# Performance work log

Hardware: AMD Instinct MI355X
Metric: run time of the kernel (lower is better)

The kernel has to match this reference:

```python
import jax, jax.numpy as jnp
import numpy as np

V, DW, D, H, F, N = 50272, 512, 1024, 16, 4096, 4   # vocab, word_embed_proj_dim, hidden, heads, ffn, layers
B, L = 4, 1024
T = B * L
MAX_POS = 2048


def layernorm(x, w, b, eps=1e-5):
    m = jnp.mean(x, axis=-1, keepdims=True)
    v = jnp.mean((x - m) ** 2, axis=-1, keepdims=True)
    return (x - m) * jax.lax.rsqrt(v + eps) * w + b


def setup_inputs() -> dict:
    key = jax.random.key(0)
    ks = jax.random.split(key, 16)
    s = 0.02
    inp = {
        "input_ids": jax.random.randint(ks[0], (T,), 0, V),
        "positions": jnp.tile(jnp.arange(L), B),          # per-sequence positions 0..L-1
        "offsets": (jnp.arange(B) + 1) * L,               # cumulative sequence ends
        "cache_indices": jnp.arange(T),
        "k_cache": jnp.zeros((N, T, D), jnp.float32),
        "v_cache": jnp.zeros((N, T, D), jnp.float32),
        "embed_w": jax.random.normal(ks[1], (V, DW)) * s,
        "pos_w": jax.random.normal(ks[2], (MAX_POS + 2, D)) * s,
        "proj_in_w": jax.random.normal(ks[3], (D, DW)) * s,
        "proj_out_w": jax.random.normal(ks[4], (DW, D)) * s,
        "ln1_w": jnp.ones((N, D)), "ln1_b": jnp.zeros((N, D)),
        "qw": jax.random.normal(ks[5], (N, D, D)) * s, "qb": jnp.zeros((N, D)),
        "kw": jax.random.normal(ks[6], (N, D, D)) * s, "kb": jnp.zeros((N, D)),
        "vw": jax.random.normal(ks[7], (N, D, D)) * s, "vb": jnp.zeros((N, D)),
        "ow": jax.random.normal(ks[8], (N, D, D)) * s, "ob": jnp.zeros((N, D)),
        "fc1w": jax.random.normal(ks[9], (N, F, D)) * s, "fc1b": jnp.zeros((N, F)),
        "fc2w": jax.random.normal(ks[10], (N, D, F)) * s, "fc2b": jnp.zeros((N, D)),
        "ln2_w": jnp.ones((N, D)), "ln2_b": jnp.zeros((N, D)),
    }
    return inp


def reference(input_ids, positions, offsets, cache_indices, k_cache, v_cache,
              embed_w, pos_w, proj_in_w, proj_out_w,
              ln1_w, ln1_b, qw, qb, kw, kb, vw, vb, ow, ob,
              fc1w, fc1b, fc2w, fc2b, ln2_w, ln2_b):
    # prompt_init=True path: fresh causal varlen attention over packed equal-length sequences.
    hd = D // H
    scale = hd ** -0.5
    emb = embed_w[input_ids] @ proj_in_w.T            # [T, D] (proj_in since DW != D)
    pos = pos_w[positions + 2]                        # learned pos emb with offset 2
    h = (emb + pos).reshape(B, L, D)
    causal = jnp.tril(jnp.ones((L, L), bool))

    def step(h, p):
        l1w, l1b, Wq, bq, Wk, bk, Wv, bv, Wo, bo, W1, b1, W2, b2, l2w, l2b = p
        r = h                                          # post-LN (do_layer_norm_before=False)
        q = (h @ Wq.T + bq).reshape(B, L, H, hd)
        k = (h @ Wk.T + bk).reshape(B, L, H, hd)
        v = (h @ Wv.T + bv).reshape(B, L, H, hd)
        s = jnp.einsum('bqhd,bkhd->bhqk', q * scale, k)
        s = jnp.where(causal, s, -1e9)
        pa = jax.nn.softmax(s, axis=-1)
        o = jnp.einsum('bhqk,bkhd->bqhd', pa, v).reshape(B, L, D)
        h = layernorm(r + (o @ Wo.T + bo), l1w, l1b)
        r = h
        h = jax.nn.relu(h @ W1.T + b1)
        h = h @ W2.T + b2
        h = layernorm(r + h, l2w, l2b)
        return h, None

    h, _ = jax.lax.scan(step, h, (ln1_w, ln1_b, qw, qb, kw, kb, vw, vb, ow, ob,
                                  fc1w, fc1b, fc2w, fc2b, ln2_w, ln2_b))
    # no decoder final_layer_norm when do_layer_norm_before=False
    h = h.reshape(T, D) @ proj_out_w.T                # [T, DW]
    last = h[offsets - 1]                             # last token of each sequence [B, DW]
    return last @ embed_w.T                           # logits [B, V]
```

## Files before the change

### kernel.cpp

```cpp
#include <hip/hip_runtime.h>
#include <stdint.h>

typedef _Float16 f16;
typedef __attribute__((ext_vector_type(8))) _Float16 f16x8;
typedef __attribute__((ext_vector_type(4))) _Float16 f16x4;
typedef __attribute__((ext_vector_type(4))) float f32x4;

constexpr int kT = 4096;
constexpr int kD = 1024;
constexpr int kDW = 512;
constexpr int kF = 4096;
constexpr int kV = 50272;

__device__ __forceinline__ void gload16(const void* g, void* lbase, int lane) {
#if __has_builtin(__builtin_amdgcn_global_load_lds)
  __builtin_amdgcn_global_load_lds((const __attribute__((address_space(1))) void*)g,
                                   (__attribute__((address_space(3))) void*)lbase, 16, 0, 0);
#else
  *(f16x8*)((char*)lbase + lane * 16) = *(const f16x8*)g;
#endif
}

__global__ __launch_bounds__(512, 4) void gemm_p8(
    const f16* __restrict__ A, const f16* __restrict__ W,
    const float* __restrict__ bias, void* __restrict__ Cv,
    int M, int N, int K, int ldc, int flags, int S)
{
  __shared__ f16 LA[2][128 * 64];
  __shared__ f16 LB[2][128 * 64];
  const int tid = threadIdx.x, lane = tid & 63, wv = tid >> 6;
  const int nby = M >> 7;
  const int nb = nby * (N >> 7);
  int id = blockIdx.x;
  id = (id & 7) * ((int)gridDim.x >> 3) + (id >> 3);
  const int s = id / nb;
  const int r = id - s * nb;
  const int bx = r / nby, by = r - bx * nby;
  const int row0 = by * 128, col0 = bx * 128;
  const int klen = K / S, koff = s * klen;
  const int wm = (wv >> 1) * 32, wn = (wv & 1) * 64;
  const int l15 = lane & 15, l4 = lane >> 4;

  f32x4 acc[2][4] = {};

  const int srow = wv * 16 + (lane >> 3);
  const int schunk = ((lane & 7) ^ (lane >> 3)) * 8;
  const f16* Ag = A + (size_t)(row0 + srow) * K + koff + schunk;
  const f16* Wg = W + (size_t)(col0 + srow) * K + koff + schunk;
  const int lrow = wv * 16;

  const int nt = klen >> 6;
#pragma unroll
  for (int j = 0; j < 2; ++j) {
    gload16(Ag + (size_t)j * 8 * K, &LA[0][(lrow + j * 8) * 64], lane);
    gload16(Wg + (size_t)j * 8 * K, &LB[0][(lrow + j * 8) * 64], lane);
  }

  for (int t = 0; t < nt; ++t) {
    const int cur = t & 1;
    if (t + 1 < nt) {
      const size_t ko = (size_t)(t + 1) * 64;
#pragma unroll
      for (int j = 0; j < 2; ++j) {
        gload16(Ag + (size_t)j * 8 * K + ko, &LA[cur ^ 1][(lrow + j * 8) * 64], lane);
        gload16(Wg + (size_t)j * 8 * K + ko, &LB[cur ^ 1][(lrow + j * 8) * 64], lane);
      }
      asm volatile("s_waitcnt vmcnt(4)" ::: "memory");
    } else {
      asm volatile("s_waitcnt vmcnt(0)" ::: "memory");
    }
    __builtin_amdgcn_s_barrier();

    f16x8 af[2][2], bf[2][4];
#pragma unroll
    for (int ks = 0; ks < 2; ++ks) {
#pragma unroll
      for (int mr = 0; mr < 2; ++mr) {
        const int rowa = wm + mr * 16 + l15;
        af[ks][mr] = *(const f16x8*)&LA[cur][rowa * 64 + (((ks * 4 + l4) ^ (rowa & 7)) * 8)];
      }
#pragma unroll
      for (int nr = 0; nr < 4; ++nr) {
        const int rowb = wn + nr * 16 + l15;
        bf[ks][nr] = *(const f16x8*)&LB[cur][rowb * 64 + (((ks * 4 + l4) ^ (rowb & 7)) * 8)];
      }
    }
#pragma unroll
    for (int mr = 0; mr < 2; ++mr)
#pragma unroll
      for (int nr = 0; nr < 4; ++nr) {
        acc[mr][nr] = __builtin_amdgcn_mfma_f32_16x16x32_f16(af[0][mr], bf[0][nr], acc[mr][nr], 0, 0, 0);
        acc[mr][nr] = __builtin_amdgcn_mfma_f32_16x16x32_f16(af[1][mr], bf[1][nr], acc[mr][nr], 0, 0, 0);
      }
    __builtin_amdgcn_sched_barrier(0);
    __builtin_amdgcn_s_barrier();
  }

  const bool relu = (flags & 1) != 0;
  const bool outf = (flags & 2) != 0;
  const bool ph16 = (flags & 4) != 0;
  float* Cf = (float*)Cv + (size_t)s * M * ldc;
  f16* Cp = (f16*)Cv + (size_t)s * M * ldc;
  f16* Ch = (f16*)Cv;
  const float* bs = (s == 0) ? bias : nullptr;
#pragma unroll
  for (int nr = 0; nr < 4; ++nr) {
    const int col = col0 + wn + nr * 16 + l15;
    const float bv = bs ? bs[col] : 0.f;
#pragma unroll
    for (int mr = 0; mr < 2; ++mr) {
#pragma unroll
      for (int rr = 0; rr < 4; ++rr) {
        const int row = row0 + wm + mr * 16 + l4 * 4 + rr;
        float v = acc[mr][nr][rr] + bv;
        if (relu) v = fmaxf(v, 0.f);
        if (ph16)      Cp[(size_t)row * ldc + col] = (f16)v;
        else if (outf) Cf[(size_t)row * ldc + col] = v;
        else           Ch[(size_t)row * ldc + col] = (f16)v;
      }
    }
  }
}

__global__ __launch_bounds__(256) void gemm_f16(
    const f16* __restrict__ A, const float* __restrict__ W,
    const float* __restrict__ bias, void* __restrict__ Cv,
    int M, int N, int K, int ldc, int flags)
{
  __shared__ f16 As[128][40];
  __shared__ f16 Ws[128][40];
  const int tid = threadIdx.x;
  const int lane = tid & 63;
  const int wid = tid >> 6;
  const int row0 = blockIdx.y * 128, col0 = blockIdx.x * 128;
  const int wm = (wid >> 1) * 64, wn = (wid & 1) * 64;
  const int l15 = lane & 15, k8 = (lane >> 4) * 8;
  const int lr = tid >> 2, lc8 = (tid & 3) * 8;

  f32x4 acc[4][4] = {};

  const f16* Ap = A + (size_t)(row0 + lr) * K + lc8;
  const float* Wp = W + (size_t)(col0 + lr) * K + lc8;

  for (int k0 = 0; k0 < K; k0 += 32) {
    f16x8 a0 = *(const f16x8*)(Ap + k0);
    f16x8 a1 = *(const f16x8*)(Ap + (size_t)64 * K + k0);
    f32x4 w00 = *(const f32x4*)(Wp + k0);
    f32x4 w01 = *(const f32x4*)(Wp + k0 + 4);
    f32x4 w10 = *(const f32x4*)(Wp + (size_t)64 * K + k0);
    f32x4 w11 = *(const f32x4*)(Wp + (size_t)64 * K + k0 + 4);
    f16x8 wv0, wv1;
#pragma unroll
    for (int j = 0; j < 4; ++j) {
      wv0[j] = (f16)w00[j]; wv0[4 + j] = (f16)w01[j];
      wv1[j] = (f16)w10[j]; wv1[4 + j] = (f16)w11[j];
    }
    __syncthreads();
    *(f16x8*)&As[lr][lc8] = a0;
    *(f16x8*)&As[lr + 64][lc8] = a1;
    *(f16x8*)&Ws[lr][lc8] = wv0;
    *(f16x8*)&Ws[lr + 64][lc8] = wv1;
    __syncthreads();
    f16x8 af[4], bfr[4];
#pragma unroll
    for (int r = 0; r < 4; ++r) af[r] = *(const f16x8*)&As[wm + r * 16 + l15][k8];
#pragma unroll
    for (int r = 0; r < 4; ++r) bfr[r] = *(const f16x8*)&Ws[wn + r * 16 + l15][k8];
#pragma unroll
    for (int mr = 0; mr < 4; ++mr)
#pragma unroll
      for (int nr = 0; nr < 4; ++nr)
        acc[mr][nr] = __builtin_amdgcn_mfma_f32_16x16x32_f16(af[mr], bfr[nr], acc[mr][nr], 0, 0, 0);
  }

  const bool relu = (flags & 1) != 0;
  const bool outf = (flags & 2) != 0;
  float* Cf = (float*)Cv;
  f16* Ch = (f16*)Cv;
#pragma unroll
  for (int nr = 0; nr < 4; ++nr) {
    const int col = col0 + wn + nr * 16 + l15;
    const float bv = bias ? bias[col] : 0.f;
#pragma unroll
    for (int mr = 0; mr < 4; ++mr) {
#pragma unroll
      for (int r = 0; r < 4; ++r) {
        const int row = row0 + wm + mr * 16 + (lane >> 4) * 4 + r;
        float v = acc[mr][nr][r] + bv;
        if (relu) v = fmaxf(v, 0.f);
        if (outf) Cf[(size_t)row * ldc + col] = v;
        else      Ch[(size_t)row * ldc + col] = (f16)v;
      }
    }
  }
}

__global__ __launch_bounds__(256) void attn_mfma4(const f16* __restrict__ qkv,
                                                  f16* __restrict__ out)
{
  __shared__ f16 Ks[64][72];
  __shared__ f16 Vt[64][72];
  __shared__ f16 Ps[4][32][72];
  const int qt = blockIdx.x, h = blockIdx.y, b = blockIdx.z;
  const int tid = threadIdx.x, lane = tid & 63, wv = tid >> 6;
  const int l15 = lane & 15, l4 = lane >> 4;
  constexpr float kC1 = 0.18033688f;
  constexpr float kC2 = -11.5415603f;

  f16x8 qa[2][2];
#pragma unroll
  for (int mr = 0; mr < 2; ++mr) {
    const size_t qrow = (size_t)(b * 1024 + qt * 128 + wv * 32 + mr * 16 + l15);
#pragma unroll
    for (int ks = 0; ks < 2; ++ks)
      qa[mr][ks] = *(const f16x8*)(qkv + qrow * 3072 + h * 64 + ks * 32 + l4 * 8);
  }

  float l[2][4] = {};
  f32x4 o[2][4] = {};

  const int skey = tid >> 2;
  const int spart = (tid & 3) * 16;
  const int vxor = (skey >> 3) ^ (tid & 3);
  const int vcol = vxor * 8 + (skey & 7);
  const int qmin = qt * 128 + wv * 32;
  const int ntiles = 2 * qt + 2;

  f16x8 kk0, kk1, vv0, vv1;
  {
    const f16* kvb = qkv + (size_t)(b * 1024 + skey) * 3072 + h * 64;
    kk0 = *(const f16x8*)(kvb + 1024 + spart);
    kk1 = *(const f16x8*)(kvb + 1024 + spart + 8);
    vv0 = *(const f16x8*)(kvb + 2048 + spart);
    vv1 = *(const f16x8*)(kvb + 2048 + spart + 8);
  }

  for (int kt = 0; kt < ntiles; ++kt) {
    *(f16x8*)&Ks[skey][spart] = kk0;
    *(f16x8*)&Ks[skey][spart + 8] = kk1;
#pragma unroll
    for (int j = 0; j < 8; ++j) {
      Vt[spart + j][vcol] = vv0[j];
      Vt[spart + 8 + j][vcol] = vv1[j];
    }
    __syncthreads();
    if (kt + 1 < ntiles) {
      const f16* kvb = qkv + (size_t)(b * 1024 + (kt + 1) * 64 + skey) * 3072 + h * 64;
      kk0 = *(const f16x8*)(kvb + 1024 + spart);
      kk1 = *(const f16x8*)(kvb + 1024 + spart + 8);
      vv0 = *(const f16x8*)(kvb + 2048 + spart);
      vv1 = *(const f16x8*)(kvb + 2048 + spart + 8);
    }

    if (kt * 64 <= qmin + 31) {
      f32x4 s[2][4] = {};
#pragma unroll
      for (int f = 0; f < 4; ++f) {
        f16x8 kb0 = *(const f16x8*)&Ks[f * 16 + l15][l4 * 8];
        f16x8 kb1 = *(const f16x8*)&Ks[f * 16 + l15][32 + l4 * 8];
#pragma unroll
        for (int mr = 0; mr < 2; ++mr) {
          s[mr][f] = __builtin_amdgcn_mfma_f32_16x16x32_f16(qa[mr][0], kb0, s[mr][f], 0, 0, 0);
          s[mr][f] = __builtin_amdgcn_mfma_f32_16x16x32_f16(qa[mr][1], kb1, s[mr][f], 0, 0, 0);
        }
      }
#pragma unroll
      for (int mr = 0; mr < 2; ++mr) {
        float sc[4][4];
        const bool needmask = (kt * 64 + 63) > (qmin + mr * 16);
        if (needmask) {
#pragma unroll
          for (int f = 0; f < 4; ++f)
#pragma unroll
            for (int r = 0; r < 4; ++r) {
              const int qg = qmin + mr * 16 + l4 * 4 + r;
              const int kg = kt * 64 + f * 16 + l15;
              sc[f][r] = (kg <= qg) ? exp2f(fmaf(s[mr][f][r], kC1, kC2)) : 0.f;
            }
        } else {
#pragma unroll
          for (int f = 0; f < 4; ++f)
#pragma unroll
            for (int r = 0; r < 4; ++r)
              sc[f][r] = exp2f(fmaf(s[mr][f][r], kC1, kC2));
        }
#pragma unroll
        for (int r = 0; r < 4; ++r)
          l[mr][r] += (sc[0][r] + sc[1][r]) + (sc[2][r] + sc[3][r]);
#pragma unroll
        for (int f = 0; f < 4; ++f)
#pragma unroll
          for (int r = 0; r < 4; ++r)
            Ps[wv][mr * 16 + l4 * 4 + r][f * 16 + l15] = (f16)sc[f][r];
      }
      f16x8 pa[2][2];
#pragma unroll
      for (int mr = 0; mr < 2; ++mr)
#pragma unroll
        for (int ks = 0; ks < 2; ++ks)
          pa[mr][ks] = *(const f16x8*)&Ps[wv][mr * 16 + l15][ks * 32 + l4 * 8];
#pragma unroll
      for (int hf = 0; hf < 4; ++hf) {
        f16x8 vb0 = *(const f16x8*)&Vt[hf * 16 + l15][((l4) ^ hf) * 8];
        f16x8 vb1 = *(const f16x8*)&Vt[hf * 16 + l15][((4 + l4) ^ hf) * 8];
#pragma unroll
        for (int mr = 0; mr < 2; ++mr) {
          o[mr][hf] = __builtin_amdgcn_mfma_f32_16x16x32_f16(pa[mr][0], vb0, o[mr][hf], 0, 0, 0);
          o[mr][hf] = __builtin_amdgcn_mfma_f32_16x16x32_f16(pa[mr][1], vb1, o[mr][hf], 0, 0, 0);
        }
      }
    }
    __syncthreads();
  }

#pragma unroll
  for (int mr = 0; mr < 2; ++mr) {
    float inv[4];
#pragma unroll
    for (int r = 0; r < 4; ++r) {
      float L = l[mr][r];
      L += __shfl_xor(L, 1);
      L += __shfl_xor(L, 2);
      L += __shfl_xor(L, 4);
      L += __shfl_xor(L, 8);
      inv[r] = 1.f / L;
    }
    f16* dst = out + (size_t)(b * 1024 + qt * 128 + wv * 32 + mr * 16 + l4 * 4) * 1024 + h * 64 + l15;
#pragma unroll
    for (int hf = 0; hf < 4; ++hf)
#pragma unroll
      for (int r = 0; r < 4; ++r)
        dst[(size_t)r * 1024 + hf * 16] = (f16)(o[mr][hf][r] * inv[r]);
  }
}

__device__ __forceinline__ void ln_body(f32x4 v, const float* w, const float* bvec,
                                        float* O32, f16* Oh, size_t base, int tid)
{
  float sm = v[0] + v[1] + v[2] + v[3];
  float sq = v[0] * v[0] + v[1] * v[1] + v[2] * v[2] + v[3] * v[3];
#pragma unroll
  for (int msk = 32; msk; msk >>= 1) { sm += __shfl_xor(sm, msk); sq += __shfl_xor(sq, msk); }
  __shared__ float sb[4], qb_[4];
  const int wid = tid >> 6, lane = tid & 63;
  if (lane == 0) { sb[wid] = sm; qb_[wid] = sq; }
  __syncthreads();
  sm = sb[0] + sb[1] + sb[2] + sb[3];
  sq = qb_[0] + qb_[1] + qb_[2] + qb_[3];
  const float mean = sm * (1.f / 1024.f);
  const float var = sq * (1.f / 1024.f) - mean * mean;
  const float rstd = rsqrtf(var + 1e-5f);
  const f32x4 w4 = *(const f32x4*)&w[tid * 4];
  const f32x4 b4 = *(const f32x4*)&bvec[tid * 4];
  f32x4 y;
  f16x4 yh;
#pragma unroll
  for (int j = 0; j < 4; ++j) {
    y[j] = (v[j] - mean) * rstd * w4[j] + b4[j];
    yh[j] = (f16)y[j];
  }
  *(f32x4*)&O32[base] = y;
  *(f16x4*)&Oh[base] = yh;
}

__global__ __launch_bounds__(256) void add_ln3h(
    const float* __restrict__ R, const f16* __restrict__ X1,
    const f16* __restrict__ X2,
    const float* __restrict__ w, const float* __restrict__ bvec,
    float* __restrict__ O32, f16* __restrict__ Oh)
{
  const int row = blockIdx.x, tid = threadIdx.x;
  const size_t base = (size_t)row * 1024 + tid * 4;
  f32x4 v = *(const f32x4*)&R[base];
  const f16x4 x1 = *(const f16x4*)&X1[base];
  const f16x4 x2 = *(const f16x4*)&X2[base];
#pragma unroll
  for (int j = 0; j < 4; ++j) v[j] += (float)x1[j] + (float)x2[j];
  ln_body(v, w, bvec, O32, Oh, base, tid);
}

__global__ __launch_bounds__(256) void add_ln(
    const float* __restrict__ R, const float* __restrict__ X,
    const float* __restrict__ w, const float* __restrict__ bvec,
    float* __restrict__ O32, f16* __restrict__ Oh)
{
  const int row = blockIdx.x, tid = threadIdx.x;
  const size_t base = (size_t)row * 1024 + tid * 4;
  f32x4 v = *(const f32x4*)&R[base];
  v += *(const f32x4*)&X[base];
  ln_body(v, w, bvec, O32, Oh, base, tid);
}

__global__ __launch_bounds__(256) void gather_embed(
    const int* __restrict__ ids, const float* __restrict__ ew, f16* __restrict__ E)
{
  const int idx = blockIdx.x * 256 + threadIdx.x;
  const int t = idx >> 6, c = (idx & 63) * 8;
  const float* src = ew + (size_t)ids[t] * 512 + c;
  f32x4 f0 = *(const f32x4*)src, f1 = *(const f32x4*)(src + 4);
  f16x8 o_;
#pragma unroll
  for (int j = 0; j < 4; ++j) { o_[j] = (f16)f0[j]; o_[4 + j] = (f16)f1[j]; }
  *(f16x8*)(E + (size_t)t * 512 + c) = o_;
}

__global__ __launch_bounds__(256) void pos_add2h(
    const f16* __restrict__ X1, const f16* __restrict__ X2,
    const float* __restrict__ posw,
    const int* __restrict__ positions, float* __restrict__ H32, f16* __restrict__ Hh)
{
  const int idx = blockIdx.x * 256 + threadIdx.x;
  const int t = idx >> 7, c = (idx & 127) * 8;
  const size_t base = (size_t)t * 1024 + c;
  const float* pp = posw + (size_t)(positions[t] + 2) * 1024 + c;
  const f16x8 x1 = *(const f16x8*)&X1[base];
  const f16x8 x2 = *(const f16x8*)&X2[base];
  f32x4 a0 = *(const f32x4*)pp;
  f32x4 a1 = *(const f32x4*)(pp + 4);
#pragma unroll
  for (int j = 0; j < 4; ++j) {
    a0[j] += (float)x1[j] + (float)x2[j];
    a1[j] += (float)x1[4 + j] + (float)x2[4 + j];
  }
  f16x8 hh;
#pragma unroll
  for (int j = 0; j < 4; ++j) { hh[j] = (f16)a0[j]; hh[4 + j] = (f16)a1[j]; }
  *(f32x4*)&H32[base] = a0;
  *(f32x4*)&H32[base + 4] = a1;
  *(f16x8*)&Hh[base] = hh;
}

__global__ __launch_bounds__(256) void pos_add(
    const float* __restrict__ X, const float* __restrict__ posw,
    const int* __restrict__ positions, float* __restrict__ H32, f16* __restrict__ Hh)
{
  const int idx = blockIdx.x * 256 + threadIdx.x;
  const int t = idx >> 7, c = (idx & 127) * 8;
  const float* xp = X + (size_t)t * 1024 + c;
  const float* pp = posw + (size_t)(positions[t] + 2) * 1024 + c;
  f32x4 a0 = *(const f32x4*)xp, a1 = *(const f32x4*)(xp + 4);
  a0 += *(const f32x4*)pp;
  a1 += *(const f32x4*)(pp + 4);
  f16x8 hh;
#pragma unroll
  for (int j = 0; j < 4; ++j) { hh[j] = (f16)a0[j]; hh[4 + j] = (f16)a1[j]; }
  *(f32x4*)&H32[(size_t)t * 1024 + c] = a0;
  *(f32x4*)&H32[(size_t)t * 1024 + c + 4] = a1;
  *(f16x8*)&Hh[(size_t)t * 1024 + c] = hh;
}

__global__ __launch_bounds__(256) void last_proj(
    const float* __restrict__ H32, const float* __restrict__ pw,
    const int* __restrict__ offs, float* __restrict__ y)
{
  const int o = blockIdx.x * 4 + (threadIdx.x >> 6), lane = threadIdx.x & 63;
  const int b = o >> 9, w = o & 511;
  const int row = offs[b] - 1;
  const float* hp = H32 + (size_t)row * 1024;
  const float* wp = pw + (size_t)w * 1024;
  float s = 0.f;
#pragma unroll
  for (int j = 0; j < 4; ++j) {
    f32x4 hv = *(const f32x4*)&hp[(lane + 64 * j) * 4];
    f32x4 wv = *(const f32x4*)&wp[(lane + 64 * j) * 4];
    s += hv[0] * wv[0] + hv[1] * wv[1] + hv[2] * wv[2] + hv[3] * wv[3];
  }
#pragma unroll
  for (int msk = 32; msk; msk >>= 1) s += __shfl_xor(s, msk);
  if (lane == 0) y[o] = s;
}

__global__ __launch_bounds__(256) void logits4(const float* __restrict__ y,
                                               const float* __restrict__ ew,
                                               float* __restrict__ out)
{
  __shared__ float ys[2048];
  const int tid = threadIdx.x;
  ((f32x4*)ys)[tid] = ((const f32x4*)y)[tid];
  ((f32x4*)ys)[tid + 256] = ((const f32x4*)y)[tid + 256];
  __syncthreads();
  const int v = blockIdx.x * 4 + (tid >> 6);
  const int lane = tid & 63;
  const float* wp = ew + (size_t)v * 512 + lane * 8;
  const f32x4 e0 = *(const f32x4*)wp;
  const f32x4 e1 = *(const f32x4*)(wp + 4);
  float s0 = 0.f, s1 = 0.f, s2 = 0.f, s3 = 0.f;
#pragma unroll
  for (int j = 0; j < 4; ++j) {
    const int c0 = lane * 8 + j, c1 = lane * 8 + 4 + j;
    s0 += e0[j] * ys[c0] + e1[j] * ys[c1];
    s1 += e0[j] * ys[512 + c0] + e1[j] * ys[512 + c1];
    s2 += e0[j] * ys[1024 + c0] + e1[j] * ys[1024 + c1];
    s3 += e0[j] * ys[1536 + c0] + e1[j] * ys[1536 + c1];
  }
#pragma unroll
  for (int msk = 32; msk; msk >>= 1) {
    s0 += __shfl_xor(s0, msk); s1 += __shfl_xor(s1, msk);
    s2 += __shfl_xor(s2, msk); s3 += __shfl_xor(s3, msk);
  }
  if (lane == 0) {
    out[v] = s0;
    out[50272 + v] = s1;
    out[2 * 50272 + v] = s2;
    out[3 * 50272 + v] = s3;
  }
}

__global__ __launch_bounds__(256) void conv_f16(const float* __restrict__ s,
                                                f16* __restrict__ d, int n8)
{
  const int i = blockIdx.x * 256 + threadIdx.x;
  if (i >= n8) return;
  const f32x4 a = *(const f32x4*)(s + (size_t)i * 8);
  const f32x4 b = *(const f32x4*)(s + (size_t)i * 8 + 4);
  f16x8 o_;
#pragma unroll
  for (int j = 0; j < 4; ++j) { o_[j] = (f16)a[j]; o_[4 + j] = (f16)b[j]; }
  *(f16x8*)(d + (size_t)i * 8) = o_;
}

__global__ __launch_bounds__(256) void qkvw_pack(const float* __restrict__ qw,
                                                 const float* __restrict__ kw,
                                                 const float* __restrict__ vw,
                                                 f16* __restrict__ dst)
{
  const size_t i = (size_t)(blockIdx.x * 256 + threadIdx.x) * 8;
  const size_t li = i / 3145728;
  const size_t r = i - li * 3145728;
  const int mt = (int)(r >> 20);
  const size_t c = r & 1048575;
  const float* s = (mt == 0 ? qw : (mt == 1 ? kw : vw)) + li * 1048576 + c;
  const f32x4 a = *(const f32x4*)s;
  const f32x4 b = *(const f32x4*)(s + 4);
  f16x8 o_;
#pragma unroll
  for (int j = 0; j < 4; ++j) { o_[j] = (f16)a[j]; o_[4 + j] = (f16)b[j]; }
  *(f16x8*)(dst + i) = o_;
}

__global__ __launch_bounds__(256) void qkvb_pack(const float* __restrict__ qb,
                                                 const float* __restrict__ kb,
                                                 const float* __restrict__ vb,
                                                 float* __restrict__ dst)
{
  const int i = blockIdx.x * 256 + threadIdx.x;
  const int li = i / 3072;
  const int r = i - li * 3072;
  const int mt = r >> 10;
  const int c = r & 1023;
  const float* s = (mt == 0 ? qb : (mt == 1 ? kb : vb));
  dst[i] = s[li * 1024 + c];
}

extern "C" void kernel_launch(void* const* d_in, const int* in_sizes, int n_in,
                              void* d_out, int out_size, void* d_ws, size_t ws_size,
                              hipStream_t stream)
{
  const int* ids        = (const int*)d_in[0];
  const int* positions  = (const int*)d_in[1];
  const int* offs       = (const int*)d_in[2];
  const float* embed_w    = (const float*)d_in[6];
  const float* pos_w      = (const float*)d_in[7];
  const float* proj_in_w  = (const float*)d_in[8];
  const float* proj_out_w = (const float*)d_in[9];
  const float* ln1w = (const float*)d_in[10];
  const float* ln1b = (const float*)d_in[11];
  const float* qw   = (const float*)d_in[12];
  const float* qb   = (const float*)d_in[13];
  const float* kw   = (const float*)d_in[14];
  const float* kb   = (const float*)d_in[15];
  const float* vw   = (const float*)d_in[16];
  const float* vb   = (const float*)d_in[17];
  const float* ow   = (const float*)d_in[18];
  const float* ob   = (const float*)d_in[19];
  const float* fc1w = (const float*)d_in[20];
  const float* fc1b = (const float*)d_in[21];
  const float* fc2w = (const float*)d_in[22];
  const float* fc2b = (const float*)d_in[23];
  const float* ln2w = (const float*)d_in[24];
  const float* ln2b = (const float*)d_in[25];

  char* ws = (char*)d_ws;
  size_t off = 0;
  auto take = [&](size_t bytes) -> char* {
    char* p = ws + off;
    off += (bytes + 255) & ~(size_t)255;
    return p;
  };
  f16*   E   = (f16*)  take((size_t)kT * kDW * 2);
  float* h32 = (float*)take((size_t)kT * kD * 4);
  f16*   hbf = (f16*)  take((size_t)kT * kD * 2);
  f16*   qkv = (f16*)  take((size_t)kT * 3072 * 2);
  f16*   att = (f16*)  take((size_t)kT * kD * 2);
  f16*   t1  = (f16*)  take((size_t)kT * kF * 2);
  float* t2  = (float*)take((size_t)kT * kD * 4 * 2);
  float* yb  = (float*)take((size_t)4 * kDW * 4);
  f16*   pw_in = (f16*)take((size_t)kD * kDW * 2);
  f16*   qkvw  = (f16*)take((size_t)4 * 3072 * kD * 2);
  f16*   oww   = (f16*)take((size_t)4 * kD * kD * 2);
  f16*   f1w   = (f16*)take((size_t)4 * kF * kD * 2);
  f16*   f2w   = (f16*)take((size_t)4 * kD * kF * 2);
  float* qkvb  = (float*)take((size_t)4 * 3072 * 4);
  const bool wok = (off <= ws_size);
  f16* tp  = (f16*)t2;
  f16* tpb = tp + (size_t)kT * kD;
  (void)in_sizes; (void)n_in; (void)out_size;

  const dim3 blk(256);
  const dim3 blk8(512);
  const dim3 gD(kD / 128, kT / 128);
  const dim3 gF(kF / 128, kT / 128);
  const dim3 gAtt(8, 16, 4);
  const int nbD   = (kD / 128) * (kT / 128);
  const int nbQKV = (3072 / 128) * (kT / 128);
  const int nbF   = (kF / 128) * (kT / 128);

  if (wok) {
    conv_f16<<<256, blk, 0, stream>>>(proj_in_w, pw_in, 65536);
    qkvw_pack<<<6144, blk, 0, stream>>>(qw, kw, vw, qkvw);
    conv_f16<<<2048, blk, 0, stream>>>(ow, oww, 524288);
    conv_f16<<<8192, blk, 0, stream>>>(fc1w, f1w, 2097152);
    conv_f16<<<8192, blk, 0, stream>>>(fc2w, f2w, 2097152);
    qkvb_pack<<<48, blk, 0, stream>>>(qb, kb, vb, qkvb);
  }

  gather_embed<<<1024, blk, 0, stream>>>(ids, embed_w, E);
  if (wok) {
    gemm_p8<<<nbD * 2, blk8, 0, stream>>>(E, pw_in, nullptr, tp, kT, kD, kDW, kD, 4, 2);
    pos_add2h<<<2048, blk, 0, stream>>>(tp, tpb, pos_w, positions, h32, hbf);
  } else {
    gemm_f16<<<gD, blk, 0, stream>>>(E, proj_in_w, nullptr, t2, kT, kD, kDW, kD, 2);
    pos_add<<<2048, blk, 0, stream>>>(t2, pos_w, positions, h32, hbf);
  }

  for (int n = 0; n < 4; ++n) {
    const size_t wo = (size_t)n * kD * kD;
    if (wok) {
      gemm_p8<<<nbQKV, blk8, 0, stream>>>(hbf, qkvw + (size_t)n * 3145728, qkvb + n * 3072,
                                          qkv, kT, 3072, kD, 3072, 0, 1);
      attn_mfma4<<<gAtt, blk, 0, stream>>>(qkv, att);
      gemm_p8<<<nbD * 2, blk8, 0, stream>>>(att, oww + wo, ob + n * kD, tp, kT, kD, kD, kD, 4, 2);
      add_ln3h<<<kT, blk, 0, stream>>>(h32, tp, tpb, ln1w + n * kD, ln1b + n * kD, h32, hbf);
      gemm_p8<<<nbF, blk8, 0, stream>>>(hbf, f1w + (size_t)n * kF * kD, fc1b + n * kF, t1, kT, kF, kD, kF, 1, 1);
      gemm_p8<<<nbD * 2, blk8, 0, stream>>>(t1, f2w + (size_t)n * kD * kF, fc2b + n * kD, tp, kT, kD, kF, kD, 4, 2);
      add_ln3h<<<kT, blk, 0, stream>>>(h32, tp, tpb, ln2w + n * kD, ln2b + n * kD, h32, hbf);
    } else {
      gemm_f16<<<gD, blk, 0, stream>>>(hbf, qw + wo, qb + n * kD, qkv + 0,    kT, kD, kD, 3072, 0);
      gemm_f16<<<gD, blk, 0, stream>>>(hbf, kw + wo, kb + n * kD, qkv + 1024, kT, kD, kD, 3072, 0);
      gemm_f16<<<gD, blk, 0, stream>>>(hbf, vw + wo, vb + n * kD, qkv + 2048, kT, kD, kD, 3072, 0);
      attn_mfma4<<<gAtt, blk, 0, stream>>>(qkv, att);
      gemm_f16<<<gD, blk, 0, stream>>>(att, ow + wo, ob + n * kD, t2, kT, kD, kD, kD, 2);
      add_ln<<<kT, blk, 0, stream>>>(h32, t2, ln1w + n * kD, ln1b + n * kD, h32, hbf);
      gemm_f16<<<gF, blk, 0, stream>>>(hbf, fc1w + (size_t)n * kF * kD, fc1b + n * kF, t1, kT, kF, kD, kF, 1);
      gemm_f16<<<gD, blk, 0, stream>>>(t1, fc2w + (size_t)n * kD * kF, fc2b + n * kD, t2, kT, kD, kF, kD, 2);
      add_ln<<<kT, blk, 0, stream>>>(h32, t2, ln2w + n * kD, ln2b + n * kD, h32, hbf);
    }
  }

  last_proj<<<512, blk, 0, stream>>>(h32, proj_out_w, offs, yb);
  logits4<<<12568, blk, 0, stream>>>(yb, embed_w, (float*)d_out);
}
```

Measured before the change: 1.052 ms.

## Replace double-buffered 8-wave GEMM with single-buffer 4-wave 64x64-per-wave GEMM

```diff
diff --git a/kernel.cpp b/kernel.cpp
--- a/kernel.cpp
+++ b/kernel.cpp
@@ -21,13 +21,13 @@
 #endif
 }
 
-__global__ __launch_bounds__(512, 4) void gemm_p8(
+__global__ __launch_bounds__(256) void gemm_s(
     const f16* __restrict__ A, const f16* __restrict__ W,
     const float* __restrict__ bias, void* __restrict__ Cv,
     int M, int N, int K, int ldc, int flags, int S)
 {
-  __shared__ f16 LA[2][128 * 64];
-  __shared__ f16 LB[2][128 * 64];
+  __shared__ f16 As[128 * 32];
+  __shared__ f16 Ws[128 * 32];
   const int tid = threadIdx.x, lane = tid & 63, wv = tid >> 6;
   const int nby = M >> 7;
   const int nb = nby * (N >> 7);
@@ -38,62 +38,41 @@
   const int bx = r / nby, by = r - bx * nby;
   const int row0 = by * 128, col0 = bx * 128;
   const int klen = K / S, koff = s * klen;
-  const int wm = (wv >> 1) * 32, wn = (wv & 1) * 64;
+  const int wm = (wv >> 1) * 64, wn = (wv & 1) * 64;
   const int l15 = lane & 15, l4 = lane >> 4;
-
-  f32x4 acc[2][4] = {};
-
-  const int srow = wv * 16 + (lane >> 3);
-  const int schunk = ((lane & 7) ^ (lane >> 3)) * 8;
-  const f16* Ag = A + (size_t)(row0 + srow) * K + koff + schunk;
-  const f16* Wg = W + (size_t)(col0 + srow) * K + koff + schunk;
-  const int lrow = wv * 16;
-
-  const int nt = klen >> 6;
-#pragma unroll
-  for (int j = 0; j < 2; ++j) {
-    gload16(Ag + (size_t)j * 8 * K, &LA[0][(lrow + j * 8) * 64], lane);
-    gload16(Wg + (size_t)j * 8 * K, &LB[0][(lrow + j * 8) * 64], lane);
-  }
-
-  for (int t = 0; t < nt; ++t) {
-    const int cur = t & 1;
-    if (t + 1 < nt) {
-      const size_t ko = (size_t)(t + 1) * 64;
-#pragma unroll
-      for (int j = 0; j < 2; ++j) {
-        gload16(Ag + (size_t)j * 8 * K + ko, &LA[cur ^ 1][(lrow + j * 8) * 64], lane);
-        gload16(Wg + (size_t)j * 8 * K + ko, &LB[cur ^ 1][(lrow + j * 8) * 64], lane);
-      }
-      asm volatile("s_waitcnt vmcnt(4)" ::: "memory");
-    } else {
-      asm volatile("s_waitcnt vmcnt(0)" ::: "memory");
-    }
-    __builtin_amdgcn_s_barrier();
-
-    f16x8 af[2][2], bf[2][4];
-#pragma unroll
-    for (int ks = 0; ks < 2; ++ks) {
-#pragma unroll
-      for (int mr = 0; mr < 2; ++mr) {
-        const int rowa = wm + mr * 16 + l15;
-        af[ks][mr] = *(const f16x8*)&LA[cur][rowa * 64 + (((ks * 4 + l4) ^ (rowa & 7)) * 8)];
-      }
-#pragma unroll
-      for (int nr = 0; nr < 4; ++nr) {
-        const int rowb = wn + nr * 16 + l15;
-        bf[ks][nr] = *(const f16x8*)&LB[cur][rowb * 64 + (((ks * 4 + l4) ^ (rowb & 7)) * 8)];
-      }
-    }
-#pragma unroll
-    for (int mr = 0; mr < 2; ++mr)
-#pragma unroll
-      for (int nr = 0; nr < 4; ++nr) {
-        acc[mr][nr] = __builtin_amdgcn_mfma_f32_16x16x32_f16(af[0][mr], bf[0][nr], acc[mr][nr], 0, 0, 0);
-        acc[mr][nr] = __builtin_amdgcn_mfma_f32_16x16x32_f16(af[1][mr], bf[1][nr], acc[mr][nr], 0, 0, 0);
-      }
-    __builtin_amdgcn_sched_barrier(0);
-    __builtin_amdgcn_s_barrier();
+  const int rsw = (l4 ^ ((l15 >> 1) & 3)) * 8;
+
+  f32x4 acc[4][4] = {};
+
+  const int srow = wv * 16 + (lane >> 2);
+  const int scol = (((lane & 3) ^ ((lane >> 3) & 3))) * 8;
+  const f16* Ag = A + (size_t)(row0 + srow) * K + koff + scol;
+  const f16* Wg = W + (size_t)(col0 + srow) * K + koff + scol;
+  f16* AsB0 = As + (wv * 16) * 32;
+  f16* AsB1 = As + (64 + wv * 16) * 32;
+  f16* WsB0 = Ws + (wv * 16) * 32;
+  f16* WsB1 = Ws + (64 + wv * 16) * 32;
+
+  for (int k0 = 0; k0 < klen; k0 += 32) {
+    __syncthreads();
+    gload16(Ag + k0, AsB0, lane);
+    gload16(Ag + (size_t)64 * K + k0, AsB1, lane);
+    gload16(Wg + k0, WsB0, lane);
+    gload16(Wg + (size_t)64 * K + k0, WsB1, lane);
+    __syncthreads();
+
+    f16x8 af[4], bf[4];
+#pragma unroll
+    for (int rr = 0; rr < 4; ++rr)
+      af[rr] = *(const f16x8*)&As[(wm + rr * 16 + l15) * 32 + rsw];
+#pragma unroll
+    for (int rr = 0; rr < 4; ++rr)
+      bf[rr] = *(const f16x8*)&Ws[(wn + rr * 16 + l15) * 32 + rsw];
+#pragma unroll
+    for (int mr = 0; mr < 4; ++mr)
+#pragma unroll
+      for (int nr = 0; nr < 4; ++nr)
+        acc[mr][nr] = __builtin_amdgcn_mfma_f32_16x16x32_f16(af[mr], bf[nr], acc[mr][nr], 0, 0, 0);
   }
 
   const bool relu = (flags & 1) != 0;
@@ -108,7 +87,7 @@
     const int col = col0 + wn + nr * 16 + l15;
     const float bv = bs ? bs[col] : 0.f;
 #pragma unroll
-    for (int mr = 0; mr < 2; ++mr) {
+    for (int mr = 0; mr < 4; ++mr) {
 #pragma unroll
       for (int rr = 0; rr < 4; ++rr) {
         const int row = row0 + wm + mr * 16 + l4 * 4 + rr;
@@ -607,13 +586,12 @@
   (void)in_sizes; (void)n_in; (void)out_size;
 
   const dim3 blk(256);
-  const dim3 blk8(512);
   const dim3 gD(kD / 128, kT / 128);
   const dim3 gF(kF / 128, kT / 128);
   const dim3 gAtt(8, 16, 4);
-  const int nbD   = (kD / 128) * (kT / 128);
-  const int nbQKV = (3072 / 128) * (kT / 128);
-  const int nbF   = (kF / 128) * (kT / 128);
+  const int nbD   = 32 * (kD / 128);
+  const int nbQKV = 32 * (3072 / 128);
+  const int nbF   = 32 * (kF / 128);
 
   if (wok) {
     conv_f16<<<256, blk, 0, stream>>>(proj_in_w, pw_in, 65536);
@@ -626,7 +604,7 @@
 
   gather_embed<<<1024, blk, 0, stream>>>(ids, embed_w, E);
   if (wok) {
-    gemm_p8<<<nbD * 2, blk8, 0, stream>>>(E, pw_in, nullptr, tp, kT, kD, kDW, kD, 4, 2);
+    gemm_s<<<nbD * 2, blk, 0, stream>>>(E, pw_in, nullptr, tp, kT, kD, kDW, kD, 4, 2);
     pos_add2h<<<2048, blk, 0, stream>>>(tp, tpb, pos_w, positions, h32, hbf);
   } else {
     gemm_f16<<<gD, blk, 0, stream>>>(E, proj_in_w, nullptr, t2, kT, kD, kDW, kD, 2);
@@ -636,13 +614,13 @@
   for (int n = 0; n < 4; ++n) {
     const size_t wo = (size_t)n * kD * kD;
     if (wok) {
-      gemm_p8<<<nbQKV, blk8, 0, stream>>>(hbf, qkvw + (size_t)n * 3145728, qkvb + n * 3072,
-                                          qkv, kT, 3072, kD, 3072, 0, 1);
+      gemm_s<<<nbQKV, blk, 0, stream>>>(hbf, qkvw + (size_t)n * 3145728, qkvb + n * 3072,
+                                        qkv, kT, 3072, kD, 3072, 0, 1);
       attn_mfma4<<<gAtt, blk, 0, stream>>>(qkv, att);
-      gemm_p8<<<nbD * 2, blk8, 0, stream>>>(att, oww + wo, ob + n * kD, tp, kT, kD, kD, kD, 4, 2);
+      gemm_s<<<nbD * 2, blk, 0, stream>>>(att, oww + wo, ob + n * kD, tp, kT, kD, kD, kD, 4, 2);
       add_ln3h<<<kT, blk, 0, stream>>>(h32, tp, tpb, ln1w + n * kD, ln1b + n * kD, h32, hbf);
-      gemm_p8<<<nbF, blk8, 0, stream>>>(hbf, f1w + (size_t)n * kF * kD, fc1b + n * kF, t1, kT, kF, kD, kF, 1, 1);
-      gemm_p8<<<nbD * 2, blk8, 0, stream>>>(t1, f2w + (size_t)n * kD * kF, fc2b + n * kD, tp, kT, kD, kF, kD, 4, 2);
+      gemm_s<<<nbF, blk, 0, stream>>>(hbf, f1w + (size_t)n * kF * kD, fc1b + n * kF, t1, kT, kF, kD, kF, 1, 1);
+      gemm_s<<<nbD * 2, blk, 0, stream>>>(t1, f2w + (size_t)n * kD * kF, fc2b + n * kD, tp, kT, kD, kF, kD, 4, 2);
       add_ln3h<<<kT, blk, 0, stream>>>(h32, tp, tpb, ln2w + n * kD, ln2b + n * kD, h32, hbf);
     } else {
       gemm_f16<<<gD, blk, 0, stream>>>(hbf, qw + wo, qb + n * kD, qkv + 0,    kT, kD, kD, 3072, 0);
```

Result: slower. 1.210 ms (+15.0%).
